# Kernel optimization log

Hardware: AMD Instinct MI355X
Metric: run time of the kernel (lower is better)

Reference implementation:

```python
import jax, jax.numpy as jnp
import numpy as np

V = 50000
E = 10000
Q = 32
F_DIM = 256
OUT_DIM = 256
B = 2


def setup_inputs() -> dict:
    key = jax.random.key(0)
    k1, k2, k3, k4 = jax.random.split(key, 4)
    X = jax.random.normal(k1, (B, V, F_DIM), dtype=jnp.float32)
    edge_nodes = jax.random.randint(k2, (E, Q), 0, V, dtype=jnp.int64)
    W = jax.random.normal(k3, (OUT_DIM, F_DIM), dtype=jnp.float32) * (1.0 / np.sqrt(F_DIM))
    b = jax.random.normal(k4, (OUT_DIM,), dtype=jnp.float32) * 0.01
    return {"X": X, "edge_nodes": edge_nodes, "W": W, "b": b}


def reference(X, edge_nodes, W, b):
    # X: [B, V, F]; edge_nodes: [E, Q] node indices per hyperedge
    Bn, Vn, Fn = X.shape
    En, Qn = edge_nodes.shape
    # gather-mean per hyperedge: agg[b,e,:] = mean_q X[b, edge_nodes[e,q], :]
    gathered = X[:, edge_nodes, :]                      # [B, E, Q, F]
    agg = gathered.mean(axis=2)                          # [B, E, F]
    flat = edge_nodes.reshape(-1)                        # [E*Q]
    # scatter-add agg back to every member node of its hyperedge
    vals = jnp.broadcast_to(agg[:, :, None, :], (Bn, En, Qn, Fn)).reshape(Bn, En * Qn, Fn)
    X_out = jnp.zeros_like(X).at[:, flat, :].add(vals)   # [B, V, F]
    # degree = number of hyperedge memberships per node, clamped to >= 1
    deg = jnp.zeros((Vn,), X.dtype).at[flat].add(1.0)
    deg = jnp.maximum(deg, 1.0)
    X_out = X_out / deg[None, :, None]
    # fc: Linear(in_dim, out_dim)
    return X_out @ W.T + b
```

## Files before the change

### kernel.cpp

```cpp
#include <hip/hip_runtime.h>
#include <hip/hip_bf16.h>
#include <stdint.h>

static constexpr int V_N = 50000;
static constexpr int E_N = 10000;
static constexpr int Q_N = 32;
static constexpr int F_N = 256;
static constexpr int SLOT_STRIDE = 40;
static constexpr int NXV = (2 * V_N * F_N) / 4;
static constexpr int NWV = (F_N * F_N) / 4;
static constexpr int T_TILES = E_N / 8;
static constexpr int LDS_STRIDE = 264;
static constexpr int PREP_GRID = 2048;

typedef unsigned short us;
typedef float f32x4 __attribute__((ext_vector_type(4)));
typedef us us4 __attribute__((ext_vector_type(4)));
typedef __bf16 bf16x8 __attribute__((ext_vector_type(8)));

__device__ __forceinline__ us f2b(float f) {
  unsigned x = __builtin_bit_cast(unsigned, f);
  x += 0x7fffu + ((x >> 16) & 1u);
  return (us)(x >> 16);
}
__device__ __forceinline__ float b2f(us u) {
  unsigned x = ((unsigned)u) << 16;
  return __builtin_bit_cast(float, x);
}


__global__ __launch_bounds__(256) void k_prep_bucket(
    const float* __restrict__ X, const float* __restrict__ Wm,
    const int* __restrict__ en, us* __restrict__ Xb, us* __restrict__ Wb,
    int* __restrict__ cnt, int* __restrict__ slots) {
  int tid = blockIdx.x * 256 + threadIdx.x;
  const int NT = PREP_GRID * 256;
  for (int i = tid; i < NXV + NWV; i += NT) {
    if (i < NXV) {
      f32x4 v = ((const f32x4*)X)[i];
      us4 o;
      #pragma unroll
      for (int j = 0; j < 4; ++j) o[j] = f2b(v[j]);
      ((us4*)Xb)[i] = o;
    } else {
      int k = i - NXV;
      f32x4 v = ((const f32x4*)Wm)[k];
      us4 o;
      #pragma unroll
      for (int j = 0; j < 4; ++j) o[j] = f2b(v[j]);
      ((us4*)Wb)[k] = o;
    }
  }
  for (int i = tid; i < E_N * Q_N; i += NT) {
    int v = en[i];
    int pos = atomicAdd(&cnt[v], 1);
    if (pos < SLOT_STRIDE) slots[v * SLOT_STRIDE + pos] = i >> 5;
  }
}


__global__ __launch_bounds__(256) void k_agg_gemm(
    const us* __restrict__ Xb, const int* __restrict__ en,
    const us* __restrict__ Wb, us* __restrict__ Yb) {
  __shared__ us tile[16 * LDS_STRIDE];
  const int t = blockIdx.x;
  const int w = threadIdx.x >> 6;
  const int lane = threadIdx.x & 63;
  const int m = lane & 15;
  const int quad = lane >> 4;
  const int col = lane * 4;

  int e0 = t * 8 + 2 * w;
  int n0 = en[e0 * Q_N + (lane & 31)];
  int n1 = en[(e0 + 1) * Q_N + (lane & 31)];
  const us* X0 = Xb + col;
  const us* X1 = Xb + (size_t)V_N * F_N + col;
  float a00[4] = {0, 0, 0, 0}, a01[4] = {0, 0, 0, 0};
  float a10[4] = {0, 0, 0, 0}, a11[4] = {0, 0, 0, 0};
  #pragma unroll 4
  for (int q = 0; q < Q_N; ++q) {
    int ma = __shfl(n0, q, 64);
    int mb = __shfl(n1, q, 64);
    us4 u0a = *(const us4*)(X0 + (size_t)ma * F_N);
    us4 u1a = *(const us4*)(X1 + (size_t)ma * F_N);
    us4 u0b = *(const us4*)(X0 + (size_t)mb * F_N);
    us4 u1b = *(const us4*)(X1 + (size_t)mb * F_N);
    #pragma unroll
    for (int j = 0; j < 4; ++j) {
      a00[j] += b2f(u0a[j]); a01[j] += b2f(u1a[j]);
      a10[j] += b2f(u0b[j]); a11[j] += b2f(u1b[j]);
    }
  }
  const float s = 1.0f / 32.0f;
  int s0 = 2 * w, s1 = 2 * w + 1;
  us4 o0, o1, o2, o3;
  #pragma unroll
  for (int j = 0; j < 4; ++j) {
    o0[j] = f2b(a00[j] * s); o1[j] = f2b(a01[j] * s);
    o2[j] = f2b(a10[j] * s); o3[j] = f2b(a11[j] * s);
  }
  *(us4*)(tile + s0 * LDS_STRIDE + col) = o0;
  *(us4*)(tile + (8 + s0) * LDS_STRIDE + col) = o1;
  *(us4*)(tile + s1 * LDS_STRIDE + col) = o2;
  *(us4*)(tile + (8 + s1) * LDS_STRIDE + col) = o3;
  __syncthreads();

  bf16x8 af[8];
  #pragma unroll
  for (int kk = 0; kk < 8; ++kk)
    af[kk] = *(const bf16x8*)(tile + m * LDS_STRIDE + quad * 8 + kk * 32);
  #pragma unroll
  for (int i = 0; i < 4; ++i) {
    int nt = w * 4 + i;
    const us* bp = Wb + (size_t)(nt * 16 + m) * F_N + quad * 8;
    f32x4 acc = {0.f, 0.f, 0.f, 0.f};
    #pragma unroll
    for (int kk = 0; kk < 8; ++kk) {
      bf16x8 bv = *(const bf16x8*)(bp + kk * 32);
      acc = __builtin_amdgcn_mfma_f32_16x16x32_bf16(af[kk], bv, acc, 0, 0, 0);
    }
    #pragma unroll
    for (int r = 0; r < 4; ++r) {
      int dr = quad * 4 + r;
      int yrow = (dr < 8) ? (t * 8 + dr) : (E_N + t * 8 + dr - 8);
      Yb[(size_t)yrow * 256 + nt * 16 + m] = f2b(acc[r]);
    }
  }
}


__global__ __launch_bounds__(256) void k_out(
    const us* __restrict__ Yb, const int* __restrict__ cnt,
    const int* __restrict__ slots, const float* __restrict__ bias,
    float* __restrict__ out) {
  int w = threadIdx.x >> 6;
  int lane = threadIdx.x & 63;
  int v = blockIdx.x * 4 + w;
  int col = lane * 4;
  int c = cnt[v];
  if (c > SLOT_STRIDE) c = SLOT_STRIDE;
  const int* sb = slots + (size_t)v * SLOT_STRIDE;
  const us* Y0 = Yb + col;
  const us* Y1 = Yb + (size_t)E_N * 256 + col;
  float acc0[4] = {0, 0, 0, 0}, acc1[4] = {0, 0, 0, 0};
  int j = 0;
  for (; j + 4 <= c; j += 4) {
    int ea = sb[j], eb = sb[j + 1], ec = sb[j + 2], ed = sb[j + 3];
    us4 pa0 = *(const us4*)(Y0 + (size_t)ea * 256);
    us4 pa1 = *(const us4*)(Y1 + (size_t)ea * 256);
    us4 pb0 = *(const us4*)(Y0 + (size_t)eb * 256);
    us4 pb1 = *(const us4*)(Y1 + (size_t)eb * 256);
    us4 pc0 = *(const us4*)(Y0 + (size_t)ec * 256);
    us4 pc1 = *(const us4*)(Y1 + (size_t)ec * 256);
    us4 pd0 = *(const us4*)(Y0 + (size_t)ed * 256);
    us4 pd1 = *(const us4*)(Y1 + (size_t)ed * 256);
    #pragma unroll
    for (int k = 0; k < 4; ++k) {
      acc0[k] += (b2f(pa0[k]) + b2f(pb0[k])) + (b2f(pc0[k]) + b2f(pd0[k]));
      acc1[k] += (b2f(pa1[k]) + b2f(pb1[k])) + (b2f(pc1[k]) + b2f(pd1[k]));
    }
  }
  for (; j < c; ++j) {
    int e = sb[j];
    us4 p0 = *(const us4*)(Y0 + (size_t)e * 256);
    us4 p1 = *(const us4*)(Y1 + (size_t)e * 256);
    #pragma unroll
    for (int k = 0; k < 4; ++k) { acc0[k] += b2f(p0[k]); acc1[k] += b2f(p1[k]); }
  }
  float inv = 1.0f / (float)(c > 0 ? c : 1);
  f32x4 bb = *(const f32x4*)(bias + col);
  f32x4 r0, r1;
  #pragma unroll
  for (int k = 0; k < 4; ++k) {
    r0[k] = bb[k] + acc0[k] * inv;
    r1[k] = bb[k] + acc1[k] * inv;
  }
  *(f32x4*)(out + (size_t)v * 256 + col) = r0;
  *(f32x4*)(out + ((size_t)V_N + v) * 256 + col) = r1;
}


extern "C" void kernel_launch(void* const* d_in, const int* in_sizes, int n_in,
                              void* d_out, int out_size, void* d_ws, size_t ws_size,
                              hipStream_t stream) {
  (void)in_sizes; (void)n_in; (void)out_size; (void)ws_size;
  const float* X = (const float*)d_in[0];
  const int* en = (const int*)d_in[1];
  const float* Wm = (const float*)d_in[2];
  const float* bias = (const float*)d_in[3];
  float* out = (float*)d_out;

  char* ws = (char*)d_ws;
  int* cnt   = (int*)(ws);
  int* slots = (int*)(ws + (1u << 20));
  us*  Wb    = (us*)(ws + (10u << 20));
  us*  Yb    = (us*)(ws + (11u << 20));
  us*  Xb    = (us*)(ws + (22u << 20));

  hipMemsetAsync(cnt, 0, V_N * sizeof(int), stream);
  k_prep_bucket<<<PREP_GRID, 256, 0, stream>>>(X, Wm, en, Xb, Wb, cnt, slots);
  k_agg_gemm<<<T_TILES, 256, 0, stream>>>(Xb, en, Wb, Yb);
  k_out<<<V_N / 4, 256, 0, stream>>>(Yb, cnt, slots, bias, out);
}
```

Before: 297.9 us.

## Interleave batch dimension in bf16 X and Y buffers and split prep work by role

X in bf16 is stored interleaved by batch, so both batch rows for a node sit next to each other, and Y rows are laid out the same way. Each gather then becomes one 16-byte load per lane instead of two 8-byte loads. The prep kernel gives separate block roles to X conversion (unrolled four ways), W conversion and degree bucketing, so the atomics run alongside the conversion. The output kernel uses nontemporal stores. The scattered index arithmetic adds a little cost, and the write pattern in prep is no longer fully contiguous.

```diff
diff --git a/kernel.cpp b/kernel.cpp
--- a/kernel.cpp
+++ b/kernel.cpp
@@ -7,15 +7,22 @@
 static constexpr int Q_N = 32;
 static constexpr int F_N = 256;
 static constexpr int SLOT_STRIDE = 40;
-static constexpr int NXV = (2 * V_N * F_N) / 4;
+static constexpr int VF4 = V_N * F_N / 4;
+static constexpr int NXV = 2 * VF4;
 static constexpr int NWV = (F_N * F_N) / 4;
 static constexpr int T_TILES = E_N / 8;
 static constexpr int LDS_STRIDE = 264;
+
 static constexpr int PREP_GRID = 2048;
+static constexpr int XBLK = 1536;
+static constexpr int XNT = XBLK * 256;
+static constexpr int WBLK = 16;
+static constexpr int BBLK = 512 - WBLK;
 
 typedef unsigned short us;
 typedef float f32x4 __attribute__((ext_vector_type(4)));
 typedef us us4 __attribute__((ext_vector_type(4)));
+typedef us us8 __attribute__((ext_vector_type(8)));
 typedef __bf16 bf16x8 __attribute__((ext_vector_type(8)));
 
 __device__ __forceinline__ us f2b(float f) {
@@ -28,33 +35,64 @@
   return __builtin_bit_cast(float, x);
 }
 
+__device__ __forceinline__ int xidx(int i) {
+  int b = (i >= VF4) ? 1 : 0;
+  int r2 = i - b * VF4;
+  return ((r2 >> 6) << 7) + (b << 6) + (r2 & 63);
+}
+
 
 __global__ __launch_bounds__(256) void k_prep_bucket(
     const float* __restrict__ X, const float* __restrict__ Wm,
     const int* __restrict__ en, us* __restrict__ Xb, us* __restrict__ Wb,
     int* __restrict__ cnt, int* __restrict__ slots) {
-  int tid = blockIdx.x * 256 + threadIdx.x;
-  const int NT = PREP_GRID * 256;
-  for (int i = tid; i < NXV + NWV; i += NT) {
-    if (i < NXV) {
+  const int bx = blockIdx.x;
+  const int r = bx & 3;
+  if (r != 3) {
+    const int tid = ((bx >> 2) * 3 + r) * 256 + (int)threadIdx.x;
+    int i = tid;
+    for (; i + 3 * XNT < NXV; i += 4 * XNT) {
+      f32x4 va = ((const f32x4*)X)[i];
+      f32x4 vb = ((const f32x4*)X)[i + XNT];
+      f32x4 vc = ((const f32x4*)X)[i + 2 * XNT];
+      f32x4 vd = ((const f32x4*)X)[i + 3 * XNT];
+      us4 oa, ob, oc, od;
+      #pragma unroll
+      for (int j = 0; j < 4; ++j) {
+        oa[j] = f2b(va[j]); ob[j] = f2b(vb[j]);
+        oc[j] = f2b(vc[j]); od[j] = f2b(vd[j]);
+      }
+      ((us4*)Xb)[xidx(i)] = oa;
+      ((us4*)Xb)[xidx(i + XNT)] = ob;
+      ((us4*)Xb)[xidx(i + 2 * XNT)] = oc;
+      ((us4*)Xb)[xidx(i + 3 * XNT)] = od;
+    }
+    for (; i < NXV; i += XNT) {
       f32x4 v = ((const f32x4*)X)[i];
       us4 o;
       #pragma unroll
       for (int j = 0; j < 4; ++j) o[j] = f2b(v[j]);
-      ((us4*)Xb)[i] = o;
+      ((us4*)Xb)[xidx(i)] = o;
+    }
+  } else {
+    const int s = bx >> 2;
+    if (s < WBLK) {
+      const int tid = s * 256 + (int)threadIdx.x;
+      for (int i = tid; i < NWV; i += WBLK * 256) {
+        f32x4 v = ((const f32x4*)Wm)[i];
+        us4 o;
+        #pragma unroll
+        for (int j = 0; j < 4; ++j) o[j] = f2b(v[j]);
+        ((us4*)Wb)[i] = o;
+      }
     } else {
-      int k = i - NXV;
-      f32x4 v = ((const f32x4*)Wm)[k];
-      us4 o;
-      #pragma unroll
-      for (int j = 0; j < 4; ++j) o[j] = f2b(v[j]);
-      ((us4*)Wb)[k] = o;
-    }
-  }
-  for (int i = tid; i < E_N * Q_N; i += NT) {
-    int v = en[i];
-    int pos = atomicAdd(&cnt[v], 1);
-    if (pos < SLOT_STRIDE) slots[v * SLOT_STRIDE + pos] = i >> 5;
+      const int tid = (s - WBLK) * 256 + (int)threadIdx.x;
+      for (int i = tid; i < E_N * Q_N; i += BBLK * 256) {
+        int v = en[i];
+        int pos = atomicAdd(&cnt[v], 1);
+        if (pos < SLOT_STRIDE) slots[v * SLOT_STRIDE + pos] = i >> 5;
+      }
+    }
   }
 }
 
@@ -68,41 +106,30 @@
   const int lane = threadIdx.x & 63;
   const int m = lane & 15;
   const int quad = lane >> 4;
-  const int col = lane * 4;
-
-  int e0 = t * 8 + 2 * w;
+  const int half = lane >> 5;
+  const int col8 = (lane & 31) * 8;
+
+  const int e0 = t * 8 + 2 * w;
   int n0 = en[e0 * Q_N + (lane & 31)];
   int n1 = en[(e0 + 1) * Q_N + (lane & 31)];
-  const us* X0 = Xb + col;
-  const us* X1 = Xb + (size_t)V_N * F_N + col;
-  float a00[4] = {0, 0, 0, 0}, a01[4] = {0, 0, 0, 0};
-  float a10[4] = {0, 0, 0, 0}, a11[4] = {0, 0, 0, 0};
+  const us* Xg = Xb + half * F_N + col8;
+  float a0[8] = {0, 0, 0, 0, 0, 0, 0, 0};
+  float a1[8] = {0, 0, 0, 0, 0, 0, 0, 0};
   #pragma unroll 4
   for (int q = 0; q < Q_N; ++q) {
     int ma = __shfl(n0, q, 64);
     int mb = __shfl(n1, q, 64);
-    us4 u0a = *(const us4*)(X0 + (size_t)ma * F_N);
-    us4 u1a = *(const us4*)(X1 + (size_t)ma * F_N);
-    us4 u0b = *(const us4*)(X0 + (size_t)mb * F_N);
-    us4 u1b = *(const us4*)(X1 + (size_t)mb * F_N);
-    #pragma unroll
-    for (int j = 0; j < 4; ++j) {
-      a00[j] += b2f(u0a[j]); a01[j] += b2f(u1a[j]);
-      a10[j] += b2f(u0b[j]); a11[j] += b2f(u1b[j]);
-    }
-  }
-  const float s = 1.0f / 32.0f;
-  int s0 = 2 * w, s1 = 2 * w + 1;
-  us4 o0, o1, o2, o3;
-  #pragma unroll
-  for (int j = 0; j < 4; ++j) {
-    o0[j] = f2b(a00[j] * s); o1[j] = f2b(a01[j] * s);
-    o2[j] = f2b(a10[j] * s); o3[j] = f2b(a11[j] * s);
-  }
-  *(us4*)(tile + s0 * LDS_STRIDE + col) = o0;
-  *(us4*)(tile + (8 + s0) * LDS_STRIDE + col) = o1;
-  *(us4*)(tile + s1 * LDS_STRIDE + col) = o2;
-  *(us4*)(tile + (8 + s1) * LDS_STRIDE + col) = o3;
+    us8 va = *(const us8*)(Xg + (size_t)ma * (2 * F_N));
+    us8 vb = *(const us8*)(Xg + (size_t)mb * (2 * F_N));
+    #pragma unroll
+    for (int j = 0; j < 8; ++j) { a0[j] += b2f(va[j]); a1[j] += b2f(vb[j]); }
+  }
+  const float sc = 1.0f / 32.0f;
+  us8 o0, o1;
+  #pragma unroll
+  for (int j = 0; j < 8; ++j) { o0[j] = f2b(a0[j] * sc); o1[j] = f2b(a1[j] * sc); }
+  *(us8*)(tile + (2 * w + 8 * half) * LDS_STRIDE + col8) = o0;
+  *(us8*)(tile + (2 * w + 1 + 8 * half) * LDS_STRIDE + col8) = o1;
   __syncthreads();
 
   bf16x8 af[8];
@@ -111,7 +138,7 @@
     af[kk] = *(const bf16x8*)(tile + m * LDS_STRIDE + quad * 8 + kk * 32);
   #pragma unroll
   for (int i = 0; i < 4; ++i) {
-    int nt = w * 4 + i;
+    const int nt = w * 4 + i;
     const us* bp = Wb + (size_t)(nt * 16 + m) * F_N + quad * 8;
     f32x4 acc = {0.f, 0.f, 0.f, 0.f};
     #pragma unroll
@@ -120,10 +147,11 @@
       acc = __builtin_amdgcn_mfma_f32_16x16x32_bf16(af[kk], bv, acc, 0, 0, 0);
     }
     #pragma unroll
-    for (int r = 0; r < 4; ++r) {
-      int dr = quad * 4 + r;
-      int yrow = (dr < 8) ? (t * 8 + dr) : (E_N + t * 8 + dr - 8);
-      Yb[(size_t)yrow * 256 + nt * 16 + m] = f2b(acc[r]);
+    for (int r2 = 0; r2 < 4; ++r2) {
+      int dr = quad * 4 + r2;
+      int e = t * 8 + (dr & 7);
+      int b = dr >> 3;
+      Yb[((size_t)e * 2 + b) * 256 + nt * 16 + m] = f2b(acc[r2]);
     }
   }
 }
@@ -133,50 +161,45 @@
     const us* __restrict__ Yb, const int* __restrict__ cnt,
     const int* __restrict__ slots, const float* __restrict__ bias,
     float* __restrict__ out) {
-  int w = threadIdx.x >> 6;
-  int lane = threadIdx.x & 63;
-  int v = blockIdx.x * 4 + w;
-  int col = lane * 4;
+  const int w = threadIdx.x >> 6;
+  const int lane = threadIdx.x & 63;
+  const int v = blockIdx.x * 4 + w;
+  const int half = lane >> 5;
+  const int col8 = (lane & 31) * 8;
   int c = cnt[v];
   if (c > SLOT_STRIDE) c = SLOT_STRIDE;
   const int* sb = slots + (size_t)v * SLOT_STRIDE;
-  const us* Y0 = Yb + col;
-  const us* Y1 = Yb + (size_t)E_N * 256 + col;
-  float acc0[4] = {0, 0, 0, 0}, acc1[4] = {0, 0, 0, 0};
+  const us* Yg = Yb + half * 256 + col8;
+  float acc[8] = {0, 0, 0, 0, 0, 0, 0, 0};
   int j = 0;
   for (; j + 4 <= c; j += 4) {
     int ea = sb[j], eb = sb[j + 1], ec = sb[j + 2], ed = sb[j + 3];
-    us4 pa0 = *(const us4*)(Y0 + (size_t)ea * 256);
-    us4 pa1 = *(const us4*)(Y1 + (size_t)ea * 256);
-    us4 pb0 = *(const us4*)(Y0 + (size_t)eb * 256);
-    us4 pb1 = *(const us4*)(Y1 + (size_t)eb * 256);
-    us4 pc0 = *(const us4*)(Y0 + (size_t)ec * 256);
-    us4 pc1 = *(const us4*)(Y1 + (size_t)ec * 256);
-    us4 pd0 = *(const us4*)(Y0 + (size_t)ed * 256);
-    us4 pd1 = *(const us4*)(Y1 + (size_t)ed * 256);
-    #pragma unroll
-    for (int k = 0; k < 4; ++k) {
-      acc0[k] += (b2f(pa0[k]) + b2f(pb0[k])) + (b2f(pc0[k]) + b2f(pd0[k]));
-      acc1[k] += (b2f(pa1[k]) + b2f(pb1[k])) + (b2f(pc1[k]) + b2f(pd1[k]));
-    }
+    us8 pa = *(const us8*)(Yg + (size_t)ea * 512);
+    us8 pb = *(const us8*)(Yg + (size_t)eb * 512);
+    us8 pc = *(const us8*)(Yg + (size_t)ec * 512);
+    us8 pd = *(const us8*)(Yg + (size_t)ed * 512);
+    #pragma unroll
+    for (int k = 0; k < 8; ++k)
+      acc[k] += (b2f(pa[k]) + b2f(pb[k])) + (b2f(pc[k]) + b2f(pd[k]));
   }
   for (; j < c; ++j) {
     int e = sb[j];
-    us4 p0 = *(const us4*)(Y0 + (size_t)e * 256);
-    us4 p1 = *(const us4*)(Y1 + (size_t)e * 256);
-    #pragma unroll
-    for (int k = 0; k < 4; ++k) { acc0[k] += b2f(p0[k]); acc1[k] += b2f(p1[k]); }
+    us8 p = *(const us8*)(Yg + (size_t)e * 512);
+    #pragma unroll
+    for (int k = 0; k < 8; ++k) acc[k] += b2f(p[k]);
   }
   float inv = 1.0f / (float)(c > 0 ? c : 1);
-  f32x4 bb = *(const f32x4*)(bias + col);
+  f32x4 b0 = *(const f32x4*)(bias + col8);
+  f32x4 b1 = *(const f32x4*)(bias + col8 + 4);
   f32x4 r0, r1;
   #pragma unroll
   for (int k = 0; k < 4; ++k) {
-    r0[k] = bb[k] + acc0[k] * inv;
-    r1[k] = bb[k] + acc1[k] * inv;
-  }
-  *(f32x4*)(out + (size_t)v * 256 + col) = r0;
-  *(f32x4*)(out + ((size_t)V_N + v) * 256 + col) = r1;
+    r0[k] = b0[k] + acc[k] * inv;
+    r1[k] = b1[k] + acc[4 + k] * inv;
+  }
+  float* op = out + ((size_t)half * V_N + v) * 256 + col8;
+  __builtin_nontemporal_store(r0, (f32x4*)op);
+  __builtin_nontemporal_store(r1, (f32x4*)(op + 4));
 }
 
 
```

Result: faster. 291.0 us (-2.3%).
